# Kernel tuning notes

Measured on AMD Instinct MI355X. Metric: run time of the kernel, lower is better.

## Reference

```python
import jax, jax.numpy as jnp
import numpy as np

B, T, D = 2, 2048, 1024
HEADS = 16
MEM = 512
HEAD_DIM = D // HEADS


def setup_inputs() -> dict:
    key = jax.random.key(0)
    k1, k2, k3, k4, k5 = jax.random.split(key, 5)
    x = jax.random.normal(k1, (B, T, D), dtype=jnp.float32)
    w_qkv = jax.random.normal(k2, (3 * D, D), dtype=jnp.float32) * (1.0 / np.sqrt(D))
    w_out = jax.random.normal(k3, (D, D), dtype=jnp.float32) * (1.0 / np.sqrt(D))
    b_out = jax.random.normal(k4, (D,), dtype=jnp.float32) * 0.01
    memory = jax.random.normal(k5, (MEM, D), dtype=jnp.float32)
    return {"x": x, "w_qkv": w_qkv, "w_out": w_out, "b_out": b_out, "memory": memory}


def reference(x, w_qkv, w_out, b_out, memory):
    b, t, d = x.shape
    h, hd = HEADS, HEAD_DIM
    scale = hd ** -0.5
    # QKV projection: [B,T,3D]
    qkv = jnp.einsum('btd,ed->bte', x, w_qkv)
    q, k, v = jnp.split(qkv, 3, axis=-1)
    # [B,H,T,hd]
    q = q.reshape(b, t, h, hd).transpose(0, 2, 1, 3)
    k = k.reshape(b, t, h, hd).transpose(0, 2, 1, 3)
    v = v.reshape(b, t, h, hd).transpose(0, 2, 1, 3)
    # memory K/V: [B,H,MEM,hd] (broadcast over batch)
    mem = memory.reshape(1, MEM, h, hd).transpose(0, 2, 1, 3)
    mem = jnp.broadcast_to(mem, (b, h, MEM, hd))
    k = jnp.concatenate([mem, k], axis=2)
    v = jnp.concatenate([mem, v], axis=2)
    # attention: scores [B,H,T,MEM+T]
    scores = jnp.einsum('bhqd,bhkd->bhqk', q, k) * scale
    weights = jax.nn.softmax(scores, axis=-1)
    out = jnp.einsum('bhqk,bhkd->bhqd', weights, v)
    out = out.transpose(0, 2, 1, 3).reshape(b, t, d)
    return jnp.einsum('btd,ed->bte', out, w_out) + b_out
```

## Files before the change

### kernel.cpp

```cpp
#include <hip/hip_runtime.h>
#include <hip/hip_bf16.h>
#include <stdint.h>

#define B_   2
#define T_   2048
#define D_   1024
#define H_   16
#define HD_  64
#define MEM_ 512
#define KV_  (MEM_ + T_)
#define NIT_ (KV_ / 64)

using bf16 = __bf16;
typedef __bf16 bf16x8 __attribute__((ext_vector_type(8)));
typedef float  f32x4  __attribute__((ext_vector_type(4)));
typedef short  s16x4  __attribute__((ext_vector_type(4)));

__device__ __forceinline__ f32x4 mfma16(bf16x8 a, bf16x8 b, f32x4 c) {
  return __builtin_amdgcn_mfma_f32_16x16x32_bf16(a, b, c, 0, 0, 0);
}
__device__ __forceinline__ f32x4 mfma16k16(s16x4 a, s16x4 b, f32x4 c) {
  return __builtin_amdgcn_mfma_f32_16x16x16bf16_1k(a, b, c, 0, 0, 0);
}

__device__ __forceinline__ void gll16(const void* g, void* l) {
  __builtin_amdgcn_global_load_lds(
      (const __attribute__((address_space(1))) unsigned int*)g,
      (__attribute__((address_space(3))) unsigned int*)l, 16, 0, 0);
}

__device__ __forceinline__ unsigned short bf16_bits(float f) {
  bf16 h = (bf16)f;
  return __builtin_bit_cast(unsigned short, h);
}

__device__ __forceinline__ ushort4 pack4(f32x4 v) {
  ushort4 p;
  p.x = bf16_bits(v[0]); p.y = bf16_bits(v[1]);
  p.z = bf16_bits(v[2]); p.w = bf16_bits(v[3]);
  return p;
}

__device__ __forceinline__ bf16x8 cvt8(f32x4 a, f32x4 b) {
  bf16x8 r;
  r[0] = (bf16)a[0]; r[1] = (bf16)a[1]; r[2] = (bf16)a[2]; r[3] = (bf16)a[3];
  r[4] = (bf16)b[0]; r[5] = (bf16)b[1]; r[6] = (bf16)b[2]; r[7] = (bf16)b[3];
  return r;
}

__global__ void prep(const float* __restrict__ x, const float* __restrict__ wq,
                     const float* __restrict__ memory,
                     bf16* __restrict__ xb, bf16* __restrict__ wqb,
                     bf16* __restrict__ mem_k, bf16* __restrict__ mem_vt) {
  int blk = blockIdx.x;
  if (blk < 3584) {
    const float* s = (blk < 2048) ? x : wq;
    bf16* d = (blk < 2048) ? xb : wqb;
    size_t i = ((size_t)(blk < 2048 ? blk : blk - 2048) * 256 + threadIdx.x) * 8;
    f32x4 a = *(const f32x4*)(s + i);
    f32x4 b = *(const f32x4*)(s + i + 4);
    *(bf16x8*)(d + i) = cvt8(a, b);
  } else {
    int idx8 = ((blk - 3584) * 256 + threadIdx.x) * 8;
    int m = idx8 >> 10, d0 = idx8 & 1023;
    int hh = d0 >> 6, hd0 = d0 & 63;
    f32x4 a = *(const f32x4*)(memory + idx8);
    f32x4 b = *(const f32x4*)(memory + idx8 + 4);
    bf16x8 r = cvt8(a, b);
    *(bf16x8*)&mem_k[((size_t)hh * MEM_ + m) * HD_ + hd0] = r;
#pragma unroll
    for (int j = 0; j < 8; j++)
      mem_vt[(size_t)(d0 + j) * MEM_ + m] = r[j];
  }
}

__global__ void conv_bf16(const float* __restrict__ s, bf16* __restrict__ d) {
  size_t i = ((size_t)blockIdx.x * 256 + threadIdx.x) * 8;
  f32x4 a = *(const f32x4*)(s + i);
  f32x4 b = *(const f32x4*)(s + i + 4);
  *(bf16x8*)(d + i) = cvt8(a, b);
}

template <int EPI, bool APLANE, int NTILE>
__global__ __launch_bounds__(256) void gemm_bt(
    const bf16* __restrict__ A, const bf16* __restrict__ W,
    const float* __restrict__ bias,
    bf16* __restrict__ q_ws, bf16* __restrict__ k_ws, bf16* __restrict__ vt_ws,
    float* __restrict__ Cout, int K) {
  constexpr int NF = NTILE / 32;
  constexpr int NB = NTILE / 32;
  __shared__ __align__(16) bf16 Als[128 * 64];
  __shared__ __align__(16) bf16 Bls[NTILE * 64];
  char* AB = (char*)Als;
  char* BB = (char*)Bls;
  const int m0 = blockIdx.y * 128;
  const int n0 = blockIdx.x * NTILE;
  const int tid = threadIdx.x;
  const int w = tid >> 6;
  const int lane = tid & 63;
  const int lx = lane & 15;
  const int quad = lane >> 4;
  const int amb = (w & 1) * 64;
  const int bnb = (w >> 1) * (NTILE / 2);
  const int srow = tid >> 3;
  const int cs = (tid & 7) ^ (srow & 7);

  f32x4 acc[4][NF];
#pragma unroll
  for (int i = 0; i < 4; i++)
#pragma unroll
    for (int j = 0; j < NF; j++) acc[i][j] = (f32x4){0.f, 0.f, 0.f, 0.f};

  for (int k0 = 0; k0 < K; k0 += 64) {
    const bf16* pa[4];
#pragma unroll
    for (int g = 0; g < 4; g++) {
      int r = srow + 32 * g;
      if constexpr (APLANE) {
        int hh = k0 >> 6, hd = cs * 8;
        int mA = m0 + r;
        pa[g] = A + ((size_t)((mA >> 11) * H_ + hh) * T_ + (mA & 2047)) * HD_ + hd;
      } else {
        pa[g] = A + (size_t)(m0 + r) * K + k0 + cs * 8;
      }
    }
    const bf16* pb[NB];
#pragma unroll
    for (int g = 0; g < NB; g++)
      pb[g] = W + (size_t)(n0 + srow + 32 * g) * K + k0 + cs * 8;

    __syncthreads();
#pragma unroll
    for (int g = 0; g < 4; g++) gll16(pa[g], AB + g * 4096 + tid * 16);
#pragma unroll
    for (int g = 0; g < NB; g++) gll16(pb[g], BB + g * 4096 + tid * 16);
    __syncthreads();

    bf16x8 af[4][2], bfr[NF][2];
    const int rk = (lx & 7) << 4;
#pragma unroll
    for (int mt = 0; mt < 4; mt++)
#pragma unroll
      for (int kh = 0; kh < 2; kh++)
        af[mt][kh] = *(const bf16x8*)(AB + (size_t)(amb + mt * 16 + lx) * 128 +
                                      ((quad * 16 + kh * 64) ^ rk));
#pragma unroll
    for (int nt = 0; nt < NF; nt++)
#pragma unroll
      for (int kh = 0; kh < 2; kh++)
        bfr[nt][kh] = *(const bf16x8*)(BB + (size_t)(bnb + nt * 16 + lx) * 128 +
                                       ((quad * 16 + kh * 64) ^ rk));
#pragma unroll
    for (int kh = 0; kh < 2; kh++)
#pragma unroll
      for (int mt = 0; mt < 4; mt++)
#pragma unroll
        for (int nt = 0; nt < NF; nt++)
          acc[mt][nt] = mfma16(af[mt][kh], bfr[nt][kh], acc[mt][nt]);
  }

  if (EPI == 0) {
#pragma unroll
    for (int mt = 0; mt < 4; mt++) {
      int mbase = m0 + amb + mt * 16 + quad * 4;
      int b = mbase >> 11;
      int t = mbase & 2047;
#pragma unroll
      for (int nt = 0; nt < NF; nt++) {
        int col = n0 + bnb + nt * 16 + lx;
        int which = col >> 10;
        int d = col & 1023;
        int hh = d >> 6, hdi = d & 63;
        int bh = b * H_ + hh;
        if (which == 0) {
#pragma unroll
          for (int r = 0; r < 4; r++)
            q_ws[((size_t)bh * T_ + t + r) * HD_ + hdi] = (bf16)acc[mt][nt][r];
        } else if (which == 1) {
#pragma unroll
          for (int r = 0; r < 4; r++)
            k_ws[((size_t)bh * T_ + t + r) * HD_ + hdi] = (bf16)acc[mt][nt][r];
        } else {
          *(ushort4*)&vt_ws[((size_t)bh * HD_ + hdi) * T_ + t] =
              pack4(acc[mt][nt]);
        }
      }
    }
  } else {
#pragma unroll
    for (int nt = 0; nt < NF; nt++) {
      int col = n0 + bnb + nt * 16 + lx;
      float bias_f = bias[col];
#pragma unroll
      for (int mt = 0; mt < 4; mt++) {
        int mbase = m0 + amb + mt * 16 + quad * 4;
#pragma unroll
        for (int r = 0; r < 4; r++)
          Cout[(size_t)(mbase + r) * D_ + col] = acc[mt][nt][r] + bias_f;
      }
    }
  }
}

__global__ __launch_bounds__(256, 2) void attn_kernel(
    bf16* __restrict__ q_ws, const bf16* __restrict__ k_ws,
    const bf16* __restrict__ vt_ws, const bf16* __restrict__ mem_k,
    const bf16* __restrict__ mem_vt) {
  __shared__ __align__(16) bf16 Kls[2 * 64 * 64];
  __shared__ __align__(16) bf16 Vls[2 * 64 * 64];
  char* KB = (char*)Kls;
  char* VB = (char*)Vls;
  const int tid = threadIdx.x;
  const int w = tid >> 6;
  const int lane = tid & 63;
  const int lx = lane & 15;
  const int quad = lane >> 4;
  const int bh = blockIdx.x & 31;
  const int qt = blockIdx.x >> 5;
  const int q0 = qt * 128 + w * 32;
  const int h = bh & 15;

  const int srow1 = tid >> 3;
  const int sc1 = (tid & 7) ^ (srow1 & 7);

  bf16* qbase = q_ws + ((size_t)bh * T_ + q0) * HD_;

  const bf16* kpl = k_ws + (size_t)bh * T_ * HD_;
  const bf16* vpl = vt_ws + (size_t)bh * HD_ * T_;
  const bf16* mkp = mem_k + (size_t)h * MEM_ * HD_;
  const bf16* mvp = mem_vt + (size_t)h * HD_ * MEM_;

  auto stage = [&](int it2, int bi) {
    const int kv0 = it2 * 64;
    const bf16 *kp1, *kp2, *vp1, *vp2;
    if (kv0 < MEM_) {
      kp1 = mkp + (size_t)(kv0 + srow1) * HD_ + sc1 * 8;
      kp2 = kp1 + (size_t)32 * HD_;
      vp1 = mvp + (size_t)srow1 * MEM_ + kv0 + sc1 * 8;
      vp2 = vp1 + (size_t)32 * MEM_;
    } else {
      const int t0 = kv0 - MEM_;
      kp1 = kpl + (size_t)(t0 + srow1) * HD_ + sc1 * 8;
      kp2 = kp1 + (size_t)32 * HD_;
      vp1 = vpl + (size_t)srow1 * T_ + t0 + sc1 * 8;
      vp2 = vp1 + (size_t)32 * T_;
    }
    char* kb = KB + bi * 8192;
    char* vb = VB + bi * 8192;
    gll16(kp1, kb + tid * 16);
    gll16(kp2, kb + tid * 16 + 4096);
    gll16(vp1, vb + tid * 16);
    gll16(vp2, vb + tid * 16 + 4096);
  };

  const float QSCALE = 0.125f * 1.44269504089f;
  bf16x8 qf[2][2];
#pragma unroll
  for (int qg = 0; qg < 2; qg++)
#pragma unroll
    for (int hf = 0; hf < 2; hf++) {
      bf16x8 v = *(const bf16x8*)(qbase + (size_t)(qg * 16 + lx) * HD_ +
                                  hf * 32 + quad * 8);
#pragma unroll
      for (int i = 0; i < 8; i++)
        v[i] = (bf16)((float)v[i] * QSCALE);
      qf[qg][hf] = v;
    }

  f32x4 o[4][2];
#pragma unroll
  for (int mt = 0; mt < 4; mt++)
#pragma unroll
    for (int qg = 0; qg < 2; qg++) o[mt][qg] = (f32x4){0.f, 0.f, 0.f, 0.f};
  float lsum[2] = {0.f, 0.f};

  stage(0, 0);

  for (int it = 0; it < NIT_; it++) {
    const int cur = it & 1;
    if (it + 1 < NIT_) {
      stage(it + 1, cur ^ 1);
      asm volatile("s_waitcnt vmcnt(4)" ::: "memory");
    } else {
      asm volatile("s_waitcnt vmcnt(0)" ::: "memory");
    }
    __builtin_amdgcn_s_barrier();
    __builtin_amdgcn_sched_barrier(0);

    const char* KBc = KB + cur * 8192;
    const char* VBc = VB + cur * 8192;
    const int sw = (lx & 7) << 4;
    f32x4 s[4][2];
    __builtin_amdgcn_s_setprio(1);
#pragma unroll
    for (int g = 0; g < 4; g++) {
      const char* kb = KBc + (size_t)(g * 16 + lx) * 128;
      bf16x8 ka0 = *(const bf16x8*)(kb + ((quad * 16) ^ sw));
      bf16x8 ka1 = *(const bf16x8*)(kb + ((64 + quad * 16) ^ sw));
#pragma unroll
      for (int qg = 0; qg < 2; qg++) {
        s[g][qg] = (f32x4){0.f, 0.f, 0.f, 0.f};
        s[g][qg] = mfma16(ka0, qf[qg][0], s[g][qg]);
        s[g][qg] = mfma16(ka1, qf[qg][1], s[g][qg]);
      }
    }
    __builtin_amdgcn_s_setprio(0);

    s16x4 pb[2][4];
#pragma unroll
    for (int qg = 0; qg < 2; qg++) {
      float ps = 0.f;
#pragma unroll
      for (int g = 0; g < 4; g++) {
#pragma unroll
        for (int r = 0; r < 4; r++) {
          float p = __builtin_amdgcn_exp2f(s[g][qg][r]);
          ps += p;
          pb[qg][g][r] = (short)bf16_bits(p);
        }
      }
      lsum[qg] += ps;
    }

    __builtin_amdgcn_s_setprio(1);
#pragma unroll
    for (int mt = 0; mt < 4; mt++) {
      const char* vb = VBc + (size_t)(mt * 16 + lx) * 128;
#pragma unroll
      for (int kk = 0; kk < 4; kk++) {
        s16x4 va = *(const s16x4*)(vb + ((kk * 32 + quad * 8) ^ sw));
#pragma unroll
        for (int qg = 0; qg < 2; qg++)
          o[mt][qg] = mfma16k16(va, pb[qg][kk], o[mt][qg]);
      }
    }
    __builtin_amdgcn_s_setprio(0);

    __builtin_amdgcn_sched_barrier(0);
    __builtin_amdgcn_s_barrier();
  }

  float inv[2];
#pragma unroll
  for (int qg = 0; qg < 2; qg++) {
    float s2 = lsum[qg];
    s2 += __shfl_xor(s2, 16);
    s2 += __shfl_xor(s2, 32);
    inv[qg] = 1.f / s2;
  }

#pragma unroll
  for (int qg = 0; qg < 2; qg++) {
#pragma unroll
    for (int mt = 0; mt < 4; mt++) {
      f32x4 ov;
#pragma unroll
      for (int r = 0; r < 4; r++) ov[r] = o[mt][qg][r] * inv[qg];
      *(ushort4*)(qbase + (size_t)(qg * 16 + lx) * HD_ + mt * 16 + quad * 4)
          = pack4(ov);
    }
  }
}

extern "C" void kernel_launch(void* const* d_in, const int* in_sizes, int n_in,
                              void* d_out, int out_size, void* d_ws,
                              size_t ws_size, hipStream_t stream) {
  const float* x      = (const float*)d_in[0];
  const float* w_qkv  = (const float*)d_in[1];
  const float* w_out  = (const float*)d_in[2];
  const float* b_out  = (const float*)d_in[3];
  const float* memory = (const float*)d_in[4];

  char* ws = (char*)d_ws;
  bf16* q_ws   = (bf16*)(ws);
  bf16* k_ws   = (bf16*)(ws + (8u << 20));
  bf16* vt_ws  = (bf16*)(ws + (16u << 20));
  bf16* mem_k  = (bf16*)(ws + (24u << 20));
  bf16* mem_vt = (bf16*)(ws + (25u << 20));
  float* out = (float*)d_out;

  char* outc = (char*)d_out;
  bf16* xb  = (bf16*)(outc);
  bf16* wqb = (bf16*)(outc + (8u << 20));
  bf16* wob = (bf16*)(ws + (8u << 20));

  prep<<<dim3(3840), dim3(256), 0, stream>>>(x, w_qkv, memory,
                                             xb, wqb, mem_k, mem_vt);
  gemm_bt<0, false, 128><<<dim3(24, 32), dim3(256), 0, stream>>>(
      xb, wqb, nullptr, q_ws, k_ws, vt_ws, nullptr, 1024);
  attn_kernel<<<dim3(512), dim3(256), 0, stream>>>(
      q_ws, k_ws, vt_ws, mem_k, mem_vt);
  conv_bf16<<<dim3(512), dim3(256), 0, stream>>>(w_out, wob);
  gemm_bt<1, true, 64><<<dim3(16, 32), dim3(256), 0, stream>>>(
      q_ws, wob, b_out, nullptr, nullptr, nullptr, out, 1024);
}
```

Before: 212.8 us.

## Use K=32 MFMA for PV, fold w_out conversion into prep, set gemm occupancy

The attention PV product now packs probabilities into 8-wide vectors and uses the 16x16x32 bf16 MFMA instead of the 16x16x16 variant, halving the number of PV MFMA instructions. The w_out bf16 conversion is merged into the prep kernel when the workspace is large enough, removing one kernel launch. The GEMM also gets a launch-bounds occupancy hint of 3 blocks per SIMD, which may constrain register allocation.

```diff
diff --git a/kernel.cpp b/kernel.cpp
--- a/kernel.cpp
+++ b/kernel.cpp
@@ -15,12 +15,10 @@
 typedef __bf16 bf16x8 __attribute__((ext_vector_type(8)));
 typedef float  f32x4  __attribute__((ext_vector_type(4)));
 typedef short  s16x4  __attribute__((ext_vector_type(4)));
+typedef short  s16x8  __attribute__((ext_vector_type(8)));
 
 __device__ __forceinline__ f32x4 mfma16(bf16x8 a, bf16x8 b, f32x4 c) {
   return __builtin_amdgcn_mfma_f32_16x16x32_bf16(a, b, c, 0, 0, 0);
-}
-__device__ __forceinline__ f32x4 mfma16k16(s16x4 a, s16x4 b, f32x4 c) {
-  return __builtin_amdgcn_mfma_f32_16x16x16bf16_1k(a, b, c, 0, 0, 0);
 }
 
 __device__ __forceinline__ void gll16(const void* g, void* l) {
@@ -50,8 +48,10 @@
 
 __global__ void prep(const float* __restrict__ x, const float* __restrict__ wq,
                      const float* __restrict__ memory,
+                     const float* __restrict__ wout,
                      bf16* __restrict__ xb, bf16* __restrict__ wqb,
-                     bf16* __restrict__ mem_k, bf16* __restrict__ mem_vt) {
+                     bf16* __restrict__ mem_k, bf16* __restrict__ mem_vt,
+                     bf16* __restrict__ wob) {
   int blk = blockIdx.x;
   if (blk < 3584) {
     const float* s = (blk < 2048) ? x : wq;
@@ -60,7 +60,7 @@
     f32x4 a = *(const f32x4*)(s + i);
     f32x4 b = *(const f32x4*)(s + i + 4);
     *(bf16x8*)(d + i) = cvt8(a, b);
-  } else {
+  } else if (blk < 3840) {
     int idx8 = ((blk - 3584) * 256 + threadIdx.x) * 8;
     int m = idx8 >> 10, d0 = idx8 & 1023;
     int hh = d0 >> 6, hd0 = d0 & 63;
@@ -71,6 +71,11 @@
 #pragma unroll
     for (int j = 0; j < 8; j++)
       mem_vt[(size_t)(d0 + j) * MEM_ + m] = r[j];
+  } else {
+    size_t i = ((size_t)(blk - 3840) * 256 + threadIdx.x) * 8;
+    f32x4 a = *(const f32x4*)(wout + i);
+    f32x4 b = *(const f32x4*)(wout + i + 4);
+    *(bf16x8*)(wob + i) = cvt8(a, b);
   }
 }
 
@@ -82,7 +87,7 @@
 }
 
 template <int EPI, bool APLANE, int NTILE>
-__global__ __launch_bounds__(256) void gemm_bt(
+__global__ __launch_bounds__(256, 3) void gemm_bt(
     const bf16* __restrict__ A, const bf16* __restrict__ W,
     const float* __restrict__ bias,
     bf16* __restrict__ q_ws, bf16* __restrict__ k_ws, bf16* __restrict__ vt_ws,
@@ -306,7 +311,7 @@
     }
     __builtin_amdgcn_s_setprio(0);
 
-    s16x4 pb[2][4];
+    s16x8 pk[2][2];
 #pragma unroll
     for (int qg = 0; qg < 2; qg++) {
       float ps = 0.f;
@@ -316,7 +321,7 @@
         for (int r = 0; r < 4; r++) {
           float p = __builtin_amdgcn_exp2f(s[g][qg][r]);
           ps += p;
-          pb[qg][g][r] = (short)bf16_bits(p);
+          pk[qg][g >> 1][(g & 1) * 4 + r] = (short)bf16_bits(p);
         }
       }
       lsum[qg] += ps;
@@ -327,11 +332,15 @@
     for (int mt = 0; mt < 4; mt++) {
       const char* vb = VBc + (size_t)(mt * 16 + lx) * 128;
 #pragma unroll
-      for (int kk = 0; kk < 4; kk++) {
-        s16x4 va = *(const s16x4*)(vb + ((kk * 32 + quad * 8) ^ sw));
+      for (int p = 0; p < 2; p++) {
+        s16x4 lo = *(const s16x4*)(vb + ((p * 64 + quad * 8) ^ sw));
+        s16x4 hi = *(const s16x4*)(vb + ((p * 64 + 32 + quad * 8) ^ sw));
+        s16x8 cat = __builtin_shufflevector(lo, hi, 0, 1, 2, 3, 4, 5, 6, 7);
+        bf16x8 va = __builtin_bit_cast(bf16x8, cat);
 #pragma unroll
         for (int qg = 0; qg < 2; qg++)
-          o[mt][qg] = mfma16k16(va, pb[qg][kk], o[mt][qg]);
+          o[mt][qg] = mfma16(va, __builtin_bit_cast(bf16x8, pk[qg][p]),
+                             o[mt][qg]);
       }
     }
     __builtin_amdgcn_s_setprio(0);
@@ -382,15 +391,19 @@
   char* outc = (char*)d_out;
   bf16* xb  = (bf16*)(outc);
   bf16* wqb = (bf16*)(outc + (8u << 20));
-  bf16* wob = (bf16*)(ws + (8u << 20));
-
-  prep<<<dim3(3840), dim3(256), 0, stream>>>(x, w_qkv, memory,
-                                             xb, wqb, mem_k, mem_vt);
+
+  const bool big_ws = ws_size >= (28u << 20);
+  bf16* wob = big_ws ? (bf16*)(ws + (26u << 20))
+                     : (bf16*)(ws + (8u << 20));
+
+  prep<<<dim3(big_ws ? 4352 : 3840), dim3(256), 0, stream>>>(
+      x, w_qkv, memory, w_out, xb, wqb, mem_k, mem_vt, wob);
   gemm_bt<0, false, 128><<<dim3(24, 32), dim3(256), 0, stream>>>(
       xb, wqb, nullptr, q_ws, k_ws, vt_ws, nullptr, 1024);
   attn_kernel<<<dim3(512), dim3(256), 0, stream>>>(
       q_ws, k_ws, vt_ws, mem_k, mem_vt);
-  conv_bf16<<<dim3(512), dim3(256), 0, stream>>>(w_out, wob);
+  if (!big_ws)
+    conv_bf16<<<dim3(512), dim3(256), 0, stream>>>(w_out, wob);
   gemm_bt<1, true, 64><<<dim3(16, 32), dim3(256), 0, stream>>>(
       q_ws, wob, b_out, nullptr, nullptr, nullptr, out, 1024);
 }
```

Measured after the change: 201.6 us. 5.2% less time.
